# Kernel optimization log

Hardware: AMD Instinct MI355X
Metric: run time of the kernel (lower is better)

Reference implementation:

```python
import jax, jax.numpy as jnp
import numpy as np

NLAYERS = 2
K = 8          # number of attention heads
H = 64         # hidden_size (per-head QK dim)
D = 1024       # input_size; value head dim = D // K = 128
B = 4
L = 1024


def setup_inputs() -> dict:
    key = jax.random.key(0)
    ks = jax.random.split(key, 5)
    s = 1.0 / np.sqrt(D).astype(np.float32)
    return {
        "x": jax.random.normal(ks[0], (B, L, D), jnp.float32),
        "Wq": jax.random.normal(ks[1], (NLAYERS, D, H * K), jnp.float32) * s,
        "bq": jnp.zeros((NLAYERS, H * K), jnp.float32),
        "Wk": jax.random.normal(ks[2], (NLAYERS, D, H * K), jnp.float32) * s,
        "bk": jnp.zeros((NLAYERS, H * K), jnp.float32),
    }


def reference(x, Wq, bq, Wk, bk):
    Bb, Ll, Dd = x.shape
    scale = 1.0 / np.sqrt(H).astype(np.float32)
    # strictly lower-triangular causal mask: torch.tril(-1)
    causal = jnp.tril(jnp.ones((Ll, Ll), x.dtype), -1)
    neg = 1e30 * (1.0 - causal)  # additive mask
    out = x
    graphs, outputs = [], []
    for i in range(NLAYERS):
        q = jax.nn.relu(out @ Wq[i] + bq[i]).reshape(Bb, Ll, K, H)
        k = jax.nn.relu(out @ Wk[i] + bk[i]).reshape(Bb, Ll, K, H)
        att = jnp.einsum('bqkh,bskh->bkqs', q, k) * scale - neg  # [B,K,L,L]
        att = jax.nn.softmax(att, axis=-1)
        v = out.reshape(Bb, Ll, K, Dd // K)                      # value = hidden itself
        cur = jnp.einsum('bkqs,bskd->bqkd', att, v).reshape(Bb, Ll, Dd)
        out = out + cur  # residual (use_gru=False)
        graphs.append(att)
        outputs.append(out)
    return jnp.stack(graphs, 0), jnp.stack(outputs, 0)
```

## Files before the change

kernel.cpp:

```cpp
#include <hip/hip_runtime.h>
#include <cstdint>
#include <cstddef>

typedef float  f32x4  __attribute__((ext_vector_type(4)));
typedef short  bf16x8 __attribute__((ext_vector_type(8)));

constexpr int Bc = 4, Lc = 1024, Dc = 1024, Kc = 8, Hc = 64, NHc = 512;
constexpr float SCALE = 0.125f;
constexpr long long GSZ = 2LL * Bc * Kc * Lc * Lc;
constexpr long long OSZ = (long long)Bc * Lc * Dc;
constexpr int QB = 16;

__device__ __forceinline__ unsigned short f2bf(float f) {
    unsigned u = __float_as_uint(f);
    u += 0x7fffu + ((u >> 16) & 1u);
    return (unsigned short)(u >> 16);
}
__device__ __forceinline__ float bf2f(unsigned short s) {
    return __uint_as_float((unsigned)s << 16);
}

__global__ __launch_bounds__(256)
void cast_bf16(const float* __restrict__ in, unsigned short* __restrict__ outp, int n)
{
    const int i = (blockIdx.x * 256 + threadIdx.x) * 8;
    if (i >= n) return;
    float4 a = *(const float4*)(in + i);
    float4 b = *(const float4*)(in + i + 4);
    bf16x8 v;
    v[0] = (short)f2bf(a.x); v[1] = (short)f2bf(a.y);
    v[2] = (short)f2bf(a.z); v[3] = (short)f2bf(a.w);
    v[4] = (short)f2bf(b.x); v[5] = (short)f2bf(b.y);
    v[6] = (short)f2bf(b.z); v[7] = (short)f2bf(b.w);
    *(bf16x8*)(outp + i) = v;
}

__global__ __launch_bounds__(256)
void wtrans(const float* __restrict__ Wq, const float* __restrict__ Wk,
            float* __restrict__ outbase)
{
    __shared__ float Tl[64][68];
    const int z = blockIdx.z, layer = z >> 1, m = z & 1;
    const float* src = (m ? Wk : Wq) + (size_t)layer * Dc * NHc;
    unsigned short* dst = (unsigned short*)(outbase + (size_t)layer * (GSZ / 2))
                          + (size_t)m * NHc * Dc;
    const int k0 = blockIdx.x * 64, n0 = blockIdx.y * 64;
    const int t = threadIdx.x;
    {
        const int r0 = t >> 4, c0 = (t & 15) * 4;
        #pragma unroll
        for (int i = 0; i < 4; ++i)
            *(float4*)&Tl[r0 + 16 * i][c0] =
                *(const float4*)&src[(size_t)(k0 + r0 + 16 * i) * NHc + n0 + c0];
    }
    __syncthreads();
    {
        const int nn = t >> 2, ks = (t & 3) * 16;
        bf16x8 v0, v1;
        #pragma unroll
        for (int j = 0; j < 8; ++j) v0[j] = (short)f2bf(Tl[ks + j][nn]);
        #pragma unroll
        for (int j = 0; j < 8; ++j) v1[j] = (short)f2bf(Tl[ks + 8 + j][nn]);
        unsigned short* dp = dst + (size_t)(n0 + nn) * Dc + k0 + ks;
        *(bf16x8*)dp       = v0;
        *(bf16x8*)(dp + 8) = v1;
    }
}

__global__ __launch_bounds__(512)
void qk_gemm(const unsigned short* __restrict__ hidb,
             const unsigned short* __restrict__ Wtq, const unsigned short* __restrict__ Wtk,
             const float* __restrict__ bq, const float* __restrict__ bk,
             unsigned short* __restrict__ qbuf, unsigned short* __restrict__ kbuf)
{
    __shared__ unsigned short As[2][128][40];
    __shared__ unsigned short Bs[2][128][40];

    const unsigned short* Wt = blockIdx.z ? Wtk : Wtq;
    const float* bi = blockIdx.z ? bk : bq;
    unsigned short* C = blockIdx.z ? kbuf : qbuf;
    const int m0 = blockIdx.x * 128, n0 = blockIdx.y * 128;
    const int t = threadIdx.x, lane = t & 63, w = t >> 6;
    const int lr = lane & 15, lg = lane >> 4;
    const int wmloc = (w >> 2) * 64, wnloc = (w & 3) * 32;

    const int srow = t >> 2, scol = (t & 3) * 8;
    const unsigned short* Ag = hidb + (size_t)(m0 + srow) * Dc + scol;
    const unsigned short* Bg = Wt   + (size_t)(n0 + srow) * Dc + scol;

    f32x4 acc[4][2] = {};
    bf16x8 ra = *(const bf16x8*)Ag;
    bf16x8 rb = *(const bf16x8*)Bg;

    for (int it = 0; it < 32; ++it) {
        const int buf = it & 1;
        *(bf16x8*)&As[buf][srow][scol] = ra;
        *(bf16x8*)&Bs[buf][srow][scol] = rb;
        __syncthreads();
        if (it < 31) {
            ra = *(const bf16x8*)(Ag + (it + 1) * 32);
            rb = *(const bf16x8*)(Bg + (it + 1) * 32);
        }
        bf16x8 a[4], bfr[2];
        #pragma unroll
        for (int mi = 0; mi < 4; ++mi)
            a[mi] = *(const bf16x8*)&As[buf][wmloc + mi * 16 + lr][lg * 8];
        #pragma unroll
        for (int ni = 0; ni < 2; ++ni)
            bfr[ni] = *(const bf16x8*)&Bs[buf][wnloc + ni * 16 + lr][lg * 8];
        #pragma unroll
        for (int mi = 0; mi < 4; ++mi)
            #pragma unroll
            for (int ni = 0; ni < 2; ++ni)
                acc[mi][ni] = __builtin_amdgcn_mfma_f32_16x16x32_bf16(a[mi], bfr[ni], acc[mi][ni], 0, 0, 0);
    }

    #pragma unroll
    for (int ni = 0; ni < 2; ++ni) {
        const int gc = n0 + wnloc + ni * 16 + lr;
        const float bv = bi[gc];
        #pragma unroll
        for (int mi = 0; mi < 4; ++mi)
            #pragma unroll
            for (int r = 0; r < 4; ++r) {
                const int row = m0 + wmloc + mi * 16 + lg * 4 + r;
                float v = fmaxf(acc[mi][ni][r] + bv, 0.0f);
                C[(size_t)row * NHc + gc] = f2bf(v);
            }
    }
}

__global__ __launch_bounds__(512)
void attn_fused(const unsigned short* __restrict__ qbuf,
                const unsigned short* __restrict__ kbuf,
                const unsigned short* __restrict__ hidb,
                const float* __restrict__ res,
                float* __restrict__ att, float* __restrict__ outp,
                unsigned short* __restrict__ hidnext)
{
    __shared__ unsigned short Sb[QB][1040];
    __shared__ unsigned short KV[2][64][132];

    const int id = blockIdx.x;
    const int kh = id & 7, qt = (id >> 3) & 63, b = id >> 9;
    const int q0 = qt * QB;
    const int t = threadIdx.x, lane = t & 63, w = t >> 6;
    const int lr = lane & 15, lg = lane >> 4;

    bf16x8 aq[2];
    #pragma unroll
    for (int ks = 0; ks < 2; ++ks)
        aq[ks] = *(const bf16x8*)(qbuf + (size_t)(b * Lc + q0 + lr) * NHc + kh * Hc + ks * 32 + lg * 8);

    const int ccount = (q0 + QB + 63) >> 6;

    const int sh = t >> 8, rr = (t & 255) >> 3, cc = (t & 7) * 8;
    for (int cb = 0; cb < ccount; cb += 2) {
        const int cs = cb + sh;
        if (cs < ccount) {
            const unsigned short* kp = kbuf + (size_t)(b * Lc + cs * 64 + rr) * NHc + kh * Hc + cc;
            *(bf16x8*)&KV[sh][rr][cc]      = *(const bf16x8*)kp;
            *(bf16x8*)&KV[sh][rr + 32][cc] = *(const bf16x8*)(kp + (size_t)32 * NHc);
        }
        __syncthreads();
        const int c = cb + (w >> 2);
        if (c < ccount) {
            const int ni = w & 3;
            f32x4 acc = {};
            __builtin_amdgcn_s_setprio(1);
            #pragma unroll
            for (int ks = 0; ks < 2; ++ks) {
                bf16x8 bfr = *(const bf16x8*)&KV[w >> 2][ni * 16 + lr][ks * 32 + lg * 8];
                acc = __builtin_amdgcn_mfma_f32_16x16x32_bf16(aq[ks], bfr, acc, 0, 0, 0);
            }
            __builtin_amdgcn_s_setprio(0);
            #pragma unroll
            for (int r = 0; r < 4; ++r)
                Sb[lg * 4 + r][c * 64 + ni * 16 + lr] = f2bf(acc[r] * SCALE);
        }
        __syncthreads();
    }

    #pragma unroll
    for (int i = 0; i < 2; ++i) {
        const int row = w * 2 + i, qrow = q0 + row;
        float* orow = att + ((size_t)(b * Kc + kh) * Lc + qrow) * Lc;
        if (qrow == 0) {
            const float u = 1.0f / 1024.0f;
            const short ub = (short)f2bf(u);
            bf16x8 pv8;
            #pragma unroll
            for (int j = 0; j < 8; ++j) pv8[j] = ub;
            #pragma unroll
            for (int tt = 0; tt < 2; ++tt) {
                const int col = lane * 8 + tt * 512;
                float4 o = { u, u, u, u };
                *(float4*)(orow + col) = o;
                *(float4*)(orow + col + 4) = o;
                *(bf16x8*)&Sb[row][col] = pv8;
            }
            continue;
        }
        float p[16];
        float mx = -3.0e38f;
        #pragma unroll
        for (int tt = 0; tt < 2; ++tt) {
            const int col = lane * 8 + tt * 512;
            bf16x8 v = *(const bf16x8*)&Sb[row][col];
            #pragma unroll
            for (int j = 0; j < 8; ++j) {
                const float f = bf2f((unsigned short)v[j]);
                p[tt * 8 + j] = f;
                if (col + j < qrow) mx = fmaxf(mx, f);
            }
        }
        #pragma unroll
        for (int off = 1; off < 64; off <<= 1) mx = fmaxf(mx, __shfl_xor(mx, off));
        float sum = 0.0f;
        #pragma unroll
        for (int tt = 0; tt < 2; ++tt)
            #pragma unroll
            for (int j = 0; j < 8; ++j) {
                const int col = lane * 8 + tt * 512 + j;
                const float e = (col < qrow) ? __expf(p[tt * 8 + j] - mx) : 0.0f;
                p[tt * 8 + j] = e; sum += e;
            }
        #pragma unroll
        for (int off = 1; off < 64; off <<= 1) sum += __shfl_xor(sum, off);
        const float inv = 1.0f / sum;
        #pragma unroll
        for (int tt = 0; tt < 2; ++tt) {
            const int col = lane * 8 + tt * 512;
            float4 o0 = { p[tt*8+0]*inv, p[tt*8+1]*inv, p[tt*8+2]*inv, p[tt*8+3]*inv };
            float4 o1 = { p[tt*8+4]*inv, p[tt*8+5]*inv, p[tt*8+6]*inv, p[tt*8+7]*inv };
            *(float4*)(orow + col) = o0;
            *(float4*)(orow + col + 4) = o1;
            bf16x8 pb;
            #pragma unroll
            for (int j = 0; j < 8; ++j) pb[j] = (short)f2bf(p[tt * 8 + j] * inv);
            *(bf16x8*)&Sb[row][col] = pb;
        }
    }
    __syncthreads();

    const int stiles = (qt == 0) ? 16 : ccount;
    f32x4 acc3 = {};
    const int dloc = w * 16 + lr, dcol = kh * 128 + dloc;
    const int vrow = t >> 3, vcol = (t & 7) * 8;
    const unsigned short* vb = hidb + (size_t)(b * Lc + vrow) * Dc + kh * 128 + vcol;
    for (int tp = 0; tp < stiles; tp += 2) {
        {
            const unsigned short* vp = vb + (size_t)tp * 64 * Dc;
            *(bf16x8*)&KV[0][vrow][vcol]      = *(const bf16x8*)vp;
            *(bf16x8*)&KV[0][vrow][vcol + 64] = *(const bf16x8*)(vp + 64);
            if (tp + 1 < stiles) {
                const unsigned short* vp1 = vp + (size_t)64 * Dc;
                *(bf16x8*)&KV[1][vrow][vcol]      = *(const bf16x8*)vp1;
                *(bf16x8*)&KV[1][vrow][vcol + 64] = *(const bf16x8*)(vp1 + 64);
            }
        }
        __syncthreads();
        __builtin_amdgcn_s_setprio(1);
        #pragma unroll
        for (int h = 0; h < 2; ++h) {
            if (tp + h < stiles) {
                #pragma unroll
                for (int ks = 0; ks < 2; ++ks) {
                    bf16x8 pa = *(const bf16x8*)&Sb[lr][(tp + h) * 64 + ks * 32 + lg * 8];
                    bf16x8 bb;
                    #pragma unroll
                    for (int j = 0; j < 8; ++j)
                        bb[j] = (short)KV[h][ks * 32 + lg * 8 + j][dloc];
                    acc3 = __builtin_amdgcn_mfma_f32_16x16x32_bf16(pa, bb, acc3, 0, 0, 0);
                }
            }
        }
        __builtin_amdgcn_s_setprio(0);
        __syncthreads();
    }

    #pragma unroll
    for (int r = 0; r < 4; ++r) {
        const size_t idx = (size_t)(b * Lc + q0 + lg * 4 + r) * Dc + dcol;
        const float v = res[idx] + acc3[r];
        outp[idx] = v;
        if (hidnext) hidnext[idx] = f2bf(v);
    }
}

extern "C" void kernel_launch(void* const* d_in, const int* in_sizes, int n_in,
                              void* d_out, int out_size, void* d_ws, size_t ws_size,
                              hipStream_t stream)
{
    const float* x  = (const float*)d_in[0];
    const float* Wq = (const float*)d_in[1];
    const float* bq = (const float*)d_in[2];
    const float* Wk = (const float*)d_in[3];
    const float* bk = (const float*)d_in[4];
    float* out = (float*)d_out;

    unsigned short* hidbA = (unsigned short*)d_ws;
    unsigned short* hidbB = hidbA + (size_t)Bc * Lc * Dc;
    unsigned short* qb    = hidbB + (size_t)Bc * Lc * Dc;
    unsigned short* kb    = qb    + (size_t)Bc * Lc * NHc;

    const int nhid = Bc * Lc * Dc;

    cast_bf16<<<nhid / 8 / 256, 256, 0, stream>>>(x, hidbA, nhid);
    wtrans<<<dim3(16, 8, 4), 256, 0, stream>>>(Wq, Wk, out);

    for (int l = 0; l < 2; ++l) {
        float* attL = out + (size_t)l * (GSZ / 2);
        float* outL = out + GSZ + (size_t)l * OSZ;
        const float* resL = l ? (out + GSZ) : x;
        const unsigned short* hidL = l ? hidbB : hidbA;
        const unsigned short* WtL = (const unsigned short*)attL;

        qk_gemm<<<dim3(32, 4, 2), 512, 0, stream>>>(
            hidL, WtL, WtL + (size_t)NHc * Dc, bq + l * NHc, bk + l * NHc, qb, kb);

        attn_fused<<<Bc * 64 * Kc, 512, 0, stream>>>(
            qb, kb, hidL, resL, attL, outL, l == 0 ? hidbB : (unsigned short*)nullptr);
    }
}
```

Measured before the change: 196.3 us.

## Double-buffer K and V tiles in LDS with register prefetch

Reworks the K-score and P·V loops of the fused attention kernel so the next tile's global loads go into registers while the current tile is computed. Each loop now alternates between two LDS buffers, which lets it drop one of its two barriers per iteration. K and V buffers share one LDS union. The V loop now handles one 64-row tile per iteration instead of two. The aim is to hide global-load latency and cut barrier stalls, at the cost of extra registers and a layout that must stay race-free with a single barrier per step.

```diff
diff --git a/kernel.cpp b/kernel.cpp
--- a/kernel.cpp
+++ b/kernel.cpp
@@ -139,7 +139,11 @@
                 unsigned short* __restrict__ hidnext)
 {
     __shared__ unsigned short Sb[QB][1040];
-    __shared__ unsigned short KV[2][64][132];
+    union KVU {
+        unsigned short KS[2][2][64][68];
+        unsigned short VT[2][64][132];
+    };
+    __shared__ KVU kv;
 
     const int id = blockIdx.x;
     const int kh = id & 7, qt = (id >> 3) & 63, b = id >> 9;
@@ -155,12 +159,24 @@
     const int ccount = (q0 + QB + 63) >> 6;
 
     const int sh = t >> 8, rr = (t & 255) >> 3, cc = (t & 7) * 8;
+    const unsigned short* kbase = kbuf + (size_t)(b * Lc + rr) * NHc + kh * Hc + cc;
+    bf16x8 kr0, kr1;
+    if (sh < ccount) {
+        const unsigned short* kp = kbase + (size_t)sh * 64 * NHc;
+        kr0 = *(const bf16x8*)kp;
+        kr1 = *(const bf16x8*)(kp + (size_t)32 * NHc);
+    }
     for (int cb = 0; cb < ccount; cb += 2) {
-        const int cs = cb + sh;
-        if (cs < ccount) {
-            const unsigned short* kp = kbuf + (size_t)(b * Lc + cs * 64 + rr) * NHc + kh * Hc + cc;
-            *(bf16x8*)&KV[sh][rr][cc]      = *(const bf16x8*)kp;
-            *(bf16x8*)&KV[sh][rr + 32][cc] = *(const bf16x8*)(kp + (size_t)32 * NHc);
+        const int buf = (cb >> 1) & 1;
+        if (cb + sh < ccount) {
+            *(bf16x8*)&kv.KS[buf][sh][rr][cc]      = kr0;
+            *(bf16x8*)&kv.KS[buf][sh][rr + 32][cc] = kr1;
+        }
+        const int nx = cb + 2 + sh;
+        if (nx < ccount) {
+            const unsigned short* kp = kbase + (size_t)nx * 64 * NHc;
+            kr0 = *(const bf16x8*)kp;
+            kr1 = *(const bf16x8*)(kp + (size_t)32 * NHc);
         }
         __syncthreads();
         const int c = cb + (w >> 2);
@@ -170,7 +186,7 @@
             __builtin_amdgcn_s_setprio(1);
             #pragma unroll
             for (int ks = 0; ks < 2; ++ks) {
-                bf16x8 bfr = *(const bf16x8*)&KV[w >> 2][ni * 16 + lr][ks * 32 + lg * 8];
+                bf16x8 bfr = *(const bf16x8*)&kv.KS[buf][w >> 2][ni * 16 + lr][ks * 32 + lg * 8];
                 acc = __builtin_amdgcn_mfma_f32_16x16x32_bf16(aq[ks], bfr, acc, 0, 0, 0);
             }
             __builtin_amdgcn_s_setprio(0);
@@ -178,8 +194,8 @@
             for (int r = 0; r < 4; ++r)
                 Sb[lg * 4 + r][c * 64 + ni * 16 + lr] = f2bf(acc[r] * SCALE);
         }
-        __syncthreads();
-    }
+    }
+    __syncthreads();
 
     #pragma unroll
     for (int i = 0; i < 2; ++i) {
@@ -248,35 +264,29 @@
     const int dloc = w * 16 + lr, dcol = kh * 128 + dloc;
     const int vrow = t >> 3, vcol = (t & 7) * 8;
     const unsigned short* vb = hidb + (size_t)(b * Lc + vrow) * Dc + kh * 128 + vcol;
-    for (int tp = 0; tp < stiles; tp += 2) {
-        {
-            const unsigned short* vp = vb + (size_t)tp * 64 * Dc;
-            *(bf16x8*)&KV[0][vrow][vcol]      = *(const bf16x8*)vp;
-            *(bf16x8*)&KV[0][vrow][vcol + 64] = *(const bf16x8*)(vp + 64);
-            if (tp + 1 < stiles) {
-                const unsigned short* vp1 = vp + (size_t)64 * Dc;
-                *(bf16x8*)&KV[1][vrow][vcol]      = *(const bf16x8*)vp1;
-                *(bf16x8*)&KV[1][vrow][vcol + 64] = *(const bf16x8*)(vp1 + 64);
-            }
+    bf16x8 vr0 = *(const bf16x8*)vb;
+    bf16x8 vr1 = *(const bf16x8*)(vb + 64);
+    for (int ti = 0; ti < stiles; ++ti) {
+        const int buf = ti & 1;
+        *(bf16x8*)&kv.VT[buf][vrow][vcol]      = vr0;
+        *(bf16x8*)&kv.VT[buf][vrow][vcol + 64] = vr1;
+        if (ti + 1 < stiles) {
+            const unsigned short* vp = vb + (size_t)(ti + 1) * 64 * Dc;
+            vr0 = *(const bf16x8*)vp;
+            vr1 = *(const bf16x8*)(vp + 64);
         }
         __syncthreads();
         __builtin_amdgcn_s_setprio(1);
         #pragma unroll
-        for (int h = 0; h < 2; ++h) {
-            if (tp + h < stiles) {
-                #pragma unroll
-                for (int ks = 0; ks < 2; ++ks) {
-                    bf16x8 pa = *(const bf16x8*)&Sb[lr][(tp + h) * 64 + ks * 32 + lg * 8];
-                    bf16x8 bb;
-                    #pragma unroll
-                    for (int j = 0; j < 8; ++j)
-                        bb[j] = (short)KV[h][ks * 32 + lg * 8 + j][dloc];
-                    acc3 = __builtin_amdgcn_mfma_f32_16x16x32_bf16(pa, bb, acc3, 0, 0, 0);
-                }
-            }
+        for (int ks = 0; ks < 2; ++ks) {
+            bf16x8 pa = *(const bf16x8*)&Sb[lr][ti * 64 + ks * 32 + lg * 8];
+            bf16x8 bb;
+            #pragma unroll
+            for (int j = 0; j < 8; ++j)
+                bb[j] = (short)kv.VT[buf][ks * 32 + lg * 8 + j][dloc];
+            acc3 = __builtin_amdgcn_mfma_f32_16x16x32_bf16(pa, bb, acc3, 0, 0, 0);
         }
         __builtin_amdgcn_s_setprio(0);
-        __syncthreads();
     }
 
     #pragma unroll
```

After: 236.1 us. 1.2x slower.
